# Kernel optimization log

Hardware: AMD Instinct MI355X
Metric: run time of the kernel (lower is better)

The kernel has to match this reference:

```python
import jax, jax.numpy as jnp
import numpy as np
import math

B, L, D, H = 4, 2048, 1024, 16
HD = D // H


def setup_inputs() -> dict:
    key = jax.random.key(0)
    k1, k2, k3 = jax.random.split(key, 3)
    x = jax.random.normal(k1, (B, L, D), dtype=jnp.float32)
    # Linear weights stored as [in, out] so y = x @ W (equivalent to torch x @ W.T)
    Wqkv = jax.random.normal(k2, (D, 3 * D), dtype=jnp.float32) * (1.0 / math.sqrt(D))
    Wproj = jax.random.normal(k3, (D, D), dtype=jnp.float32) * (1.0 / math.sqrt(D))
    attn_mask = jnp.tril(jnp.ones((L, L), dtype=bool))  # True = attend (causal)
    key_padding_mask = jnp.zeros((B, L), dtype=bool)     # True = padded (none here)
    return {"x": x, "Wqkv": Wqkv, "Wproj": Wproj,
            "attn_mask": attn_mask, "key_padding_mask": key_padding_mask}


def reference(x, Wqkv, Wproj, attn_mask, key_padding_mask):
    Bx, Lx, Dx = x.shape
    qkv = x @ Wqkv                              # [B, L, 3D]
    q, k, v = jnp.split(qkv, 3, axis=-1)
    def shape(t):
        return t.reshape(Bx, Lx, H, HD).transpose(0, 2, 1, 3)  # [B, H, L, hd]
    q, k, v = shape(q), shape(k), shape(v)
    att = jnp.einsum('bhqd,bhkd->bhqk', q, k) / math.sqrt(HD)  # [B, H, L, L]
    neg_inf = jnp.float32(-jnp.inf)
    att = jnp.where(attn_mask[None, None, :, :], att, neg_inf)
    att = jnp.where(key_padding_mask[:, None, None, :], neg_inf, att)
    att = jax.nn.softmax(att, axis=-1)
    y = jnp.einsum('bhqk,bhkd->bhqd', att, v)   # [B, H, L, hd]
    y = y.transpose(0, 2, 1, 3).reshape(Bx, Lx, Dx)
    return y @ Wproj
```

## Files before the change

### kernel.cpp

```cpp
#include <hip/hip_runtime.h>
#include <cstdint>
#include <cstddef>


typedef __attribute__((ext_vector_type(8))) __bf16 bf16x8;
typedef __attribute__((ext_vector_type(4))) __bf16 bf16x4;
typedef __attribute__((ext_vector_type(4))) float f32x4;
typedef __attribute__((ext_vector_type(16))) float f32x16;

__device__ __forceinline__ f32x4 mfma_bf16(bf16x8 a, bf16x8 b, f32x4 c) {
  return __builtin_amdgcn_mfma_f32_16x16x32_bf16(a, b, c, 0, 0, 0);
}

__device__ __forceinline__ f32x16 mfma32(bf16x8 a, bf16x8 b, f32x16 c) {
  return __builtin_amdgcn_mfma_f32_32x32x16_bf16(a, b, c, 0, 0, 0);
}

__device__ __forceinline__ unsigned cvtpk(float a, float b) {
  unsigned r;
  asm("v_cvt_pk_bf16_f32 %0, %1, %2" : "=v"(r) : "v"(a), "v"(b));
  return r;
}

__device__ __forceinline__ void async_copy16(const void* gsrc, void* ldsdst) {
  __builtin_amdgcn_global_load_lds(
      (const __attribute__((address_space(1))) void*)gsrc,
      (__attribute__((address_space(3))) void*)ldsdst, 16, 0, 0);
}

__global__ __launch_bounds__(256) void f32_to_bf16(
    const float* __restrict__ in, __bf16* __restrict__ out) {
  const size_t i = ((size_t)blockIdx.x * 256 + threadIdx.x) * 4;
  const float4 v = *(const float4*)&in[i];
  bf16x4 o = {(__bf16)v.x, (__bf16)v.y, (__bf16)v.z, (__bf16)v.w};
  *(bf16x4*)&out[i] = o;
}

__global__ __launch_bounds__(256) void transpose_f32_bf16(
    const float* __restrict__ in, __bf16* __restrict__ out, int R, int C) {
  __shared__ float tile[32][33];
  const int c0 = blockIdx.x * 32;
  const int r0 = blockIdx.y * 32;
  const int tx = threadIdx.x & 31;
  const int ty = threadIdx.x >> 5;
#pragma unroll
  for (int i = 0; i < 32; i += 8)
    tile[ty + i][tx] = in[(size_t)(r0 + ty + i) * C + c0 + tx];
  __syncthreads();
#pragma unroll
  for (int i = 0; i < 32; i += 8)
    out[(size_t)(c0 + ty + i) * R + r0 + tx] = (__bf16)tile[tx][ty + i];
}

__global__ __launch_bounds__(256) void gemm_bt_f32out(
    const __bf16* __restrict__ A, const __bf16* __restrict__ BT,
    float* __restrict__ C, int M, int N, int K) {
  __shared__ __bf16 As[128 * 32];
  __shared__ __bf16 Bs[128 * 32];
  const int tid = threadIdx.x;
  const int wave = tid >> 6;
  const int lane = tid & 63;
  const int n16 = lane & 15;
  const int quad = lane >> 4;
  const int m0 = blockIdx.x * 128;
  const int n0 = blockIdx.y * 128;
  const int wr = wave >> 1;
  const int wc = wave & 1;

  const f32x4 zero = {0.f, 0.f, 0.f, 0.f};
  f32x4 acc[4][4];
#pragma unroll
  for (int i = 0; i < 4; ++i)
#pragma unroll
    for (int j = 0; j < 4; ++j) acc[i][j] = zero;

  const int KT = K >> 5;
  for (int kt = 0; kt < KT; ++kt) {
    const int k0 = kt << 5;
#pragma unroll
    for (int r = 0; r < 2; ++r) {
      const int li = (r << 8) + tid;
      const int row = li >> 2;
      const int kp8 = (li & 3) << 3;
      const int lbase = ((r << 8) + (wave << 6)) << 3;
      async_copy16(&A[(size_t)(m0 + row) * K + k0 + kp8], &As[lbase]);
      async_copy16(&BT[(size_t)(n0 + row) * K + k0 + kp8], &Bs[lbase]);
    }
    __syncthreads();
    bf16x8 af[4], bf[4];
#pragma unroll
    for (int t = 0; t < 4; ++t) {
      af[t] = *(const bf16x8*)&As[(wr * 64 + t * 16 + n16) * 32 + quad * 8];
      bf[t] = *(const bf16x8*)&Bs[(wc * 64 + t * 16 + n16) * 32 + quad * 8];
    }
#pragma unroll
    for (int mt = 0; mt < 4; ++mt)
#pragma unroll
      for (int nt = 0; nt < 4; ++nt)
        acc[mt][nt] = mfma_bf16(af[mt], bf[nt], acc[mt][nt]);
    __syncthreads();
  }
#pragma unroll
  for (int mt = 0; mt < 4; ++mt) {
#pragma unroll
    for (int r = 0; r < 4; ++r) {
      const int m = m0 + wr * 64 + mt * 16 + quad * 4 + r;
#pragma unroll
      for (int nt = 0; nt < 4; ++nt) {
        const int n = n0 + wc * 64 + nt * 16 + n16;
        C[(size_t)m * N + n] = acc[mt][nt][r];
      }
    }
  }
}

__global__ __launch_bounds__(512, 2) void gemm_qkv(
    const __bf16* __restrict__ A, const __bf16* __restrict__ BT,
    __bf16* __restrict__ Q, __bf16* __restrict__ Kh, __bf16* __restrict__ VT) {
  extern __shared__ __bf16 smem[];
  const int K = 1024;
  const int wg = (blockIdx.x & 7) * 48 + (blockIdx.x >> 3);
  const int bm = wg / 12;
  const int bn = wg % 12;
  const int m0 = bm << 8;
  const int n0 = bn << 8;

  const int tid = threadIdx.x;
  const int wave = tid >> 6;
  const int lane = tid & 63;
  const int n16 = lane & 15;
  const int quad = lane >> 4;
  const int wr = wave >> 2;
  const int wc = wave & 3;

  const int srow = wave * 8 + (lane >> 3);
  const int schunk = ((lane & 7) ^ ((lane >> 3) & 7)) << 3;
  const __bf16* aS = &A[(size_t)(m0 + srow) * K + schunk];
  const __bf16* bS = &BT[(size_t)(n0 + srow) * K + schunk];
  __bf16* dstW = smem + wave * 512;

  const f32x4 zero = {0.f, 0.f, 0.f, 0.f};
  f32x4 acc[8][4];
#pragma unroll
  for (int i = 0; i < 8; ++i)
#pragma unroll
    for (int j = 0; j < 4; ++j) acc[i][j] = zero;

#pragma unroll
  for (int i = 0; i < 4; ++i) {
    async_copy16(aS + (size_t)i * 65536, dstW + i * 4096);
    async_copy16(bS + (size_t)i * 65536, dstW + 16384 + i * 4096);
  }

  for (int t = 0; t < 16; ++t) {
    const int base = (t & 1) << 15;
    asm volatile("s_waitcnt vmcnt(0)" ::: "memory");
    __builtin_amdgcn_s_barrier();
    if (t + 1 < 16) {
      const int nbase = ((t + 1) & 1) << 15;
      const __bf16* aT = aS + (t + 1) * 64;
      const __bf16* bT = bS + (t + 1) * 64;
#pragma unroll
      for (int i = 0; i < 4; ++i) {
        async_copy16(aT + (size_t)i * 65536, dstW + nbase + i * 4096);
        async_copy16(bT + (size_t)i * 65536, dstW + nbase + 16384 + i * 4096);
      }
    }
    const __bf16* As = smem + base;
    const __bf16* Bs = smem + base + 16384;
    bf16x8 bfr[4][2];
#pragma unroll
    for (int g = 0; g < 4; ++g)
#pragma unroll
      for (int kk = 0; kk < 2; ++kk) {
        const int row = wc * 64 + g * 16 + n16;
        const int phys = ((kk * 4 + quad) ^ (n16 & 7)) << 3;
        bfr[g][kk] = *(const bf16x8*)&Bs[row * 64 + phys];
      }
#pragma unroll
    for (int q = 0; q < 4; ++q) {
      bf16x8 afr[2][2];
#pragma unroll
      for (int fi = 0; fi < 2; ++fi)
#pragma unroll
        for (int kk = 0; kk < 2; ++kk) {
          const int row = wr * 128 + (2 * q + fi) * 16 + n16;
          const int phys = ((kk * 4 + quad) ^ (n16 & 7)) << 3;
          afr[fi][kk] = *(const bf16x8*)&As[row * 64 + phys];
        }
      __builtin_amdgcn_s_barrier();
      asm volatile("s_waitcnt lgkmcnt(0)" ::: "memory");
      __builtin_amdgcn_sched_barrier(0);
      __builtin_amdgcn_s_setprio(1);
#pragma unroll
      for (int fi = 0; fi < 2; ++fi)
#pragma unroll
        for (int g = 0; g < 4; ++g)
#pragma unroll
          for (int kk = 0; kk < 2; ++kk)
            acc[2 * q + fi][g] =
                mfma_bf16(afr[fi][kk], bfr[g][kk], acc[2 * q + fi][g]);
      __builtin_amdgcn_s_setprio(0);
      __builtin_amdgcn_s_barrier();
    }
  }

  __bf16* tw = smem + wave * 2048;
  const int b = m0 >> 11;
  const int l0w = (m0 & 2047) + wr * 128;
  const int n = n0 + wc * 64;

  if (n < 2048) {
    const float QSCALE = 0.125f * 1.44269504089f;
    const bool isQ = (n < 1024);
    const int h = (n & 1023) >> 6;
    __bf16* dst = isQ ? Q : Kh;
    const size_t bbase = ((size_t)(b * 16 + h) * 2048) * 64;
#pragma unroll
    for (int p = 0; p < 4; ++p) {
#pragma unroll
      for (int fi = 0; fi < 2; ++fi) {
        const int f = 2 * p + fi;
#pragma unroll
        for (int g = 0; g < 4; ++g)
#pragma unroll
          for (int r = 0; r < 4; ++r) {
            const int hd = g * 16 + n16;
            const int mm = fi * 16 + quad * 4 + r;
            const float v = isQ ? acc[f][g][r] * QSCALE : acc[f][g][r];
            tw[mm * 64 + (((hd >> 3) ^ (mm & 7)) << 3) + (hd & 7)] =
                (__bf16)v;
          }
      }
#pragma unroll
      for (int i = 0; i < 4; ++i) {
        const int c = lane + 64 * i;
        const int row = c >> 3;
        const int hd0 = (c & 7) << 3;
        const int phys = (c & 7) ^ (row & 7);
        const bf16x8 v = *(const bf16x8*)&tw[row * 64 + phys * 8];
        *(bf16x8*)&dst[bbase + (size_t)(l0w + p * 32 + row) * 64 + hd0] = v;
      }
    }
  } else {
    const int h = (n - 2048) >> 6;
    const size_t bhead = (size_t)(b * 16 + h);
#pragma unroll
    for (int ph = 0; ph < 2; ++ph)
#pragma unroll
      for (int lh = 0; lh < 2; ++lh) {
#pragma unroll
        for (int gi = 0; gi < 2; ++gi) {
          const int g = 2 * ph + gi;
#pragma unroll
          for (int fi = 0; fi < 4; ++fi) {
            const int f = 4 * lh + fi;
#pragma unroll
            for (int r = 0; r < 4; ++r) {
              const int hdp = gi * 16 + n16;
              const int mm = fi * 16 + quad * 4 + r;
              const int phys = (mm >> 3) ^ (hdp & 7);
              tw[hdp * 64 + phys * 8 + (mm & 7)] = (__bf16)acc[f][g][r];
            }
          }
        }
#pragma unroll
        for (int i = 0; i < 4; ++i) {
          const int c = lane + 64 * i;
          const int row = c >> 3;
          const int phys = (c & 7) ^ (row & 7);
          const bf16x8 v = *(const bf16x8*)&tw[row * 64 + phys * 8];
          *(bf16x8*)&VT[(bhead * 64 + ph * 32 + row) * 2048 + l0w + lh * 64 +
                        (c & 7) * 8] = v;
        }
      }
  }
}

__global__ __launch_bounds__(256, 2) void flash_attn(
    const __bf16* __restrict__ Q, const __bf16* __restrict__ Kh,
    const __bf16* __restrict__ VT, __bf16* __restrict__ Y) {
  __shared__ __bf16 Ks[2][64 * 64];
  __shared__ __bf16 Vs[2][64 * 64];
  const int bh = blockIdx.x;
  const int p = blockIdx.y;
  const int tid = threadIdx.x;
  const int wave = tid >> 6;
  const int lane = tid & 63;
  const int lrow = lane & 31;
  const int hi = lane >> 5;
  const int lswz = lane & 7;
  const __bf16* Qb = Q + (size_t)bh * 2048 * 64;
  const __bf16* Kb = Kh + (size_t)bh * 2048 * 64;
  const __bf16* Vb = VT + (size_t)bh * 64 * 2048;
  const int b = bh >> 4;
  const int h = bh & 15;
  const f32x16 zero16 = {0.f, 0.f, 0.f, 0.f, 0.f, 0.f, 0.f, 0.f,
                         0.f, 0.f, 0.f, 0.f, 0.f, 0.f, 0.f, 0.f};

  const int srow = tid >> 3;
  const int sswz = ((tid & 7) ^ (srow & 7)) << 3;
  const size_t kg0 = (size_t)srow * 64 + sswz;
  const size_t kg1 = (size_t)(srow + 32) * 64 + sswz;
  const size_t vg0 = (size_t)srow * 2048 + sswz;
  const size_t vg1 = (size_t)(srow + 32) * 2048 + sswz;
  const int ldst0 = wave * 512;
  const int ldst1 = 2048 + wave * 512;

#pragma unroll
  for (int tt = 0; tt < 2; ++tt) {
    const int t = tt ? 15 - p : p;
    const int q0w = t * 128 + wave * 32;
    const int myq = q0w + lrow;

    bf16x8 qf[4];
#pragma unroll
    for (int i = 0; i < 4; ++i)
      qf[i] = *(const bf16x8*)&Qb[(size_t)myq * 64 + i * 16 + hi * 8];

    f32x16 o0 = zero16, o1 = zero16;
    float lsum = 0.f;
    const int nsteps = 2 * (t + 1);

    __syncthreads();
    async_copy16(&Kb[kg0], &Ks[0][ldst0]);
    async_copy16(&Kb[kg1], &Ks[0][ldst1]);
    async_copy16(&Vb[vg0], &Vs[0][ldst0]);
    async_copy16(&Vb[vg1], &Vs[0][ldst1]);

    for (int kt = 0; kt < nsteps; ++kt) {
      const int buf = kt & 1;
      const int c0 = kt << 6;
      __syncthreads();
      if (kt + 1 < nsteps) {
        const int nb = buf ^ 1;
        const int cn = c0 + 64;
        async_copy16(&Kb[kg0 + (size_t)cn * 64], &Ks[nb][ldst0]);
        async_copy16(&Kb[kg1 + (size_t)cn * 64], &Ks[nb][ldst1]);
        async_copy16(&Vb[vg0 + cn], &Vs[nb][ldst0]);
        async_copy16(&Vb[vg1 + cn], &Vs[nb][ldst1]);
      }
      if (c0 > q0w + 31) continue;

      const __bf16* ks = Ks[buf];
      const __bf16* vs = Vs[buf];

      f32x16 sc[2];
#pragma unroll
      for (int ch = 0; ch < 2; ++ch) {
        sc[ch] = zero16;
#pragma unroll
        for (int i = 0; i < 4; ++i) {
          const bf16x8 kf = *(const bf16x8*)&ks[(ch * 32 + lrow) * 64 +
                                                (((2 * i + hi) ^ lswz) << 3)];
          sc[ch] = mfma32(kf, qf[i], sc[ch]);
        }
      }
      if (c0 + 63 > q0w) {
#pragma unroll
        for (int ch = 0; ch < 2; ++ch)
#pragma unroll
          for (int r = 0; r < 16; ++r) {
            const int k = c0 + ch * 32 + (r & 3) + 8 * (r >> 2) + 4 * hi;
            float e = __builtin_amdgcn_exp2f(sc[ch][r]);
            e = (k <= myq) ? e : 0.f;
            sc[ch][r] = e;
            lsum += e;
          }
      } else {
#pragma unroll
        for (int ch = 0; ch < 2; ++ch)
#pragma unroll
          for (int r = 0; r < 16; ++r) {
            const float e = __builtin_amdgcn_exp2f(sc[ch][r]);
            sc[ch][r] = e;
            lsum += e;
          }
      }
#pragma unroll
      for (int ch = 0; ch < 2; ++ch) {
#pragma unroll
        for (int kc = 0; kc < 2; ++kc) {
          unsigned c01 = cvtpk(sc[ch][kc * 8 + 0], sc[ch][kc * 8 + 1]);
          unsigned c23 = cvtpk(sc[ch][kc * 8 + 2], sc[ch][kc * 8 + 3]);
          unsigned c45 = cvtpk(sc[ch][kc * 8 + 4], sc[ch][kc * 8 + 5]);
          unsigned c67 = cvtpk(sc[ch][kc * 8 + 6], sc[ch][kc * 8 + 7]);
          asm("v_permlane32_swap_b32 %0, %1" : "+v"(c01), "+v"(c45));
          asm("v_permlane32_swap_b32 %0, %1" : "+v"(c23), "+v"(c67));
          union {
            unsigned u[4];
            bf16x8 v;
          } pu;
          pu.u[0] = c01;
          pu.u[1] = c23;
          pu.u[2] = c45;
          pu.u[3] = c67;
          const int kch = ch * 4 + kc * 2 + hi;
          {
            const bf16x8 vf0 = *(const bf16x8*)&vs[(0 * 32 + lrow) * 64 +
                                                   ((kch ^ lswz) << 3)];
            o0 = mfma32(pu.v, vf0, o0);
            const bf16x8 vf1 = *(const bf16x8*)&vs[(1 * 32 + lrow) * 64 +
                                                   ((kch ^ lswz) << 3)];
            o1 = mfma32(pu.v, vf1, o1);
          }
        }
      }
    }

    lsum += __shfl_xor(lsum, 32);
    const float inv = 1.0f / lsum;
    float invr[16];
#pragma unroll
    for (int r = 0; r < 16; ++r)
      invr[r] = __shfl(inv, (r & 3) + 8 * (r >> 2) + 4 * hi);
#pragma unroll
    for (int r = 0; r < 16; ++r) {
      const int row = q0w + (r & 3) + 8 * (r >> 2) + 4 * hi;
      const size_t yb = (size_t)(b * 2048 + row) * 1024 + h * 64;
      Y[yb + lrow] = (__bf16)(o0[r] * invr[r]);
      Y[yb + 32 + lrow] = (__bf16)(o1[r] * invr[r]);
    }
  }
}

extern "C" void kernel_launch(void* const* d_in, const int* in_sizes, int n_in,
                              void* d_out, int out_size, void* d_ws,
                              size_t ws_size, hipStream_t stream) {
  const float* x = (const float*)d_in[0];
  const float* Wqkv = (const float*)d_in[1];
  const float* Wproj = (const float*)d_in[2];
  float* out = (float*)d_out;

  char* ws = (char*)d_ws;
  __bf16* xb = (__bf16*)ws;     ws += (size_t)8192 * 1024 * 2;
  __bf16* WqkvT = (__bf16*)ws;  ws += (size_t)3072 * 1024 * 2;
  __bf16* WprojT = (__bf16*)ws; ws += (size_t)1024 * 1024 * 2;
  __bf16* Qs = (__bf16*)ws;     ws += (size_t)64 * 2048 * 64 * 2;
  __bf16* Ks = (__bf16*)ws;     ws += (size_t)64 * 2048 * 64 * 2;
  __bf16* VTs = (__bf16*)ws;    ws += (size_t)64 * 64 * 2048 * 2;
  __bf16* attn = xb;

  static bool attrSet = false;
  if (!attrSet) {
    hipFuncSetAttribute((const void*)gemm_qkv,
                        hipFuncAttributeMaxDynamicSharedMemorySize, 131072);
    attrSet = true;
  }

  f32_to_bf16<<<8192, 256, 0, stream>>>(x, xb);
  transpose_f32_bf16<<<dim3(96, 32), 256, 0, stream>>>(Wqkv, WqkvT, 1024, 3072);
  transpose_f32_bf16<<<dim3(32, 32), 256, 0, stream>>>(Wproj, WprojT, 1024, 1024);
  gemm_qkv<<<384, 512, 131072, stream>>>(xb, WqkvT, Qs, Ks, VTs);
  flash_attn<<<dim3(64, 8), 256, 0, stream>>>(Qs, Ks, VTs, attn);
  gemm_bt_f32out<<<dim3(64, 8), 256, 0, stream>>>(attn, WprojT, out,
                                                  8192, 1024, 1024);
}
```

Measured before the change: 253.1 us.

## Interleave global-to-LDS prefetch with MFMA phases in QKV GEMM main loop

```diff
diff --git a/kernel.cpp b/kernel.cpp
--- a/kernel.cpp
+++ b/kernel.cpp
@@ -114,6 +114,40 @@
   }
 }
 
+#define DS_B(Bs_)                                                            \
+  _Pragma("unroll") for (int g = 0; g < 4; ++g)                              \
+      _Pragma("unroll") for (int kk = 0; kk < 2; ++kk) bfr[g][kk] =          \
+          *(const bf16x8*)&(Bs_)[(wc * 64 + g * 16 + n16) * 64 +             \
+                                 (((kk * 4 + quad) ^ (n16 & 7)) << 3)];
+
+#define DS_A2(As_, q_)                                                       \
+  _Pragma("unroll") for (int fi = 0; fi < 2; ++fi)                           \
+      _Pragma("unroll") for (int kk = 0; kk < 2; ++kk) af[fi][kk] =          \
+          *(const bf16x8*)&(As_)[(wr * 128 + (2 * (q_) + fi) * 16 + n16) *   \
+                                     64 +                                    \
+                                 (((kk * 4 + quad) ^ (n16 & 7)) << 3)];
+
+#define MFMA_BODY(q_)                                                        \
+  __builtin_amdgcn_s_barrier();                                              \
+  asm volatile("s_waitcnt lgkmcnt(0)" ::: "memory");                         \
+  __builtin_amdgcn_sched_barrier(0);                                         \
+  __builtin_amdgcn_s_setprio(1);                                             \
+  _Pragma("unroll") for (int fi = 0; fi < 2; ++fi)                           \
+      _Pragma("unroll") for (int g = 0; g < 4; ++g)                          \
+          _Pragma("unroll") for (int kk = 0; kk < 2; ++kk)                   \
+              acc[2 * (q_) + fi][g] =                                        \
+      mfma_bf16(af[fi][kk], bfr[g][kk], acc[2 * (q_) + fi][g]);              \
+  __builtin_amdgcn_s_setprio(0);
+
+#define MFMA_PH(q_)                                                          \
+  MFMA_BODY(q_)                                                              \
+  __builtin_amdgcn_s_barrier();
+
+#define MFMA_PH_VM(q_)                                                       \
+  MFMA_BODY(q_)                                                              \
+  asm volatile("s_waitcnt vmcnt(6)" ::: "memory");                           \
+  __builtin_amdgcn_s_barrier();
+
 __global__ __launch_bounds__(512, 2) void gemm_qkv(
     const __bf16* __restrict__ A, const __bf16* __restrict__ BT,
     __bf16* __restrict__ Q, __bf16* __restrict__ Kh, __bf16* __restrict__ VT) {
@@ -133,11 +167,19 @@
   const int wr = wave >> 2;
   const int wc = wave & 3;
 
-  const int srow = wave * 8 + (lane >> 3);
-  const int schunk = ((lane & 7) ^ ((lane >> 3) & 7)) << 3;
-  const __bf16* aS = &A[(size_t)(m0 + srow) * K + schunk];
-  const __bf16* bS = &BT[(size_t)(n0 + srow) * K + schunk];
-  __bf16* dstW = smem + wave * 512;
+  const int srow = tid >> 3;
+  const int schunk = ((tid & 7) ^ (srow & 7)) << 3;
+  const __bf16* aBase = &A[(size_t)(m0 + srow) * K + schunk];
+  const __bf16* bBase = &BT[(size_t)(n0 + srow) * K + schunk];
+
+  auto stgA = [&](int kt, int u, int half) {
+    async_copy16(aBase + (size_t)u * 65536 + kt * 64,
+                 smem + half * 32768 + u * 4096 + wave * 512);
+  };
+  auto stgB = [&](int kt, int u, int half) {
+    async_copy16(bBase + (size_t)u * 65536 + kt * 64,
+                 smem + half * 32768 + 16384 + u * 4096 + wave * 512);
+  };
 
   const f32x4 zero = {0.f, 0.f, 0.f, 0.f};
   f32x4 acc[8][4];
@@ -146,64 +188,54 @@
 #pragma unroll
     for (int j = 0; j < 4; ++j) acc[i][j] = zero;
 
-#pragma unroll
-  for (int i = 0; i < 4; ++i) {
-    async_copy16(aS + (size_t)i * 65536, dstW + i * 4096);
-    async_copy16(bS + (size_t)i * 65536, dstW + 16384 + i * 4096);
-  }
-
-  for (int t = 0; t < 16; ++t) {
-    const int base = (t & 1) << 15;
-    asm volatile("s_waitcnt vmcnt(0)" ::: "memory");
-    __builtin_amdgcn_s_barrier();
-    if (t + 1 < 16) {
-      const int nbase = ((t + 1) & 1) << 15;
-      const __bf16* aT = aS + (t + 1) * 64;
-      const __bf16* bT = bS + (t + 1) * 64;
-#pragma unroll
-      for (int i = 0; i < 4; ++i) {
-        async_copy16(aT + (size_t)i * 65536, dstW + nbase + i * 4096);
-        async_copy16(bT + (size_t)i * 65536, dstW + nbase + 16384 + i * 4096);
-      }
-    }
-    const __bf16* As = smem + base;
-    const __bf16* Bs = smem + base + 16384;
-    bf16x8 bfr[4][2];
-#pragma unroll
-    for (int g = 0; g < 4; ++g)
-#pragma unroll
-      for (int kk = 0; kk < 2; ++kk) {
-        const int row = wc * 64 + g * 16 + n16;
-        const int phys = ((kk * 4 + quad) ^ (n16 & 7)) << 3;
-        bfr[g][kk] = *(const bf16x8*)&Bs[row * 64 + phys];
-      }
-#pragma unroll
-    for (int q = 0; q < 4; ++q) {
-      bf16x8 afr[2][2];
-#pragma unroll
-      for (int fi = 0; fi < 2; ++fi)
-#pragma unroll
-        for (int kk = 0; kk < 2; ++kk) {
-          const int row = wr * 128 + (2 * q + fi) * 16 + n16;
-          const int phys = ((kk * 4 + quad) ^ (n16 & 7)) << 3;
-          afr[fi][kk] = *(const bf16x8*)&As[row * 64 + phys];
-        }
-      __builtin_amdgcn_s_barrier();
-      asm volatile("s_waitcnt lgkmcnt(0)" ::: "memory");
-      __builtin_amdgcn_sched_barrier(0);
-      __builtin_amdgcn_s_setprio(1);
-#pragma unroll
-      for (int fi = 0; fi < 2; ++fi)
-#pragma unroll
-        for (int g = 0; g < 4; ++g)
-#pragma unroll
-          for (int kk = 0; kk < 2; ++kk)
-            acc[2 * q + fi][g] =
-                mfma_bf16(afr[fi][kk], bfr[g][kk], acc[2 * q + fi][g]);
-      __builtin_amdgcn_s_setprio(0);
-      __builtin_amdgcn_s_barrier();
-    }
-  }
+  const __bf16* As0 = smem;
+  const __bf16* Bs0 = smem + 16384;
+  const __bf16* As1 = smem + 32768;
+  const __bf16* Bs1 = smem + 49152;
+
+  stgB(0, 0, 0); stgB(0, 1, 0); stgB(0, 2, 0); stgB(0, 3, 0);
+  stgA(0, 0, 0); stgA(0, 2, 0); stgA(0, 1, 0); stgA(0, 3, 0);
+  stgB(1, 0, 1); stgB(1, 1, 1); stgB(1, 2, 1); stgB(1, 3, 1);
+  stgA(1, 0, 1); stgA(1, 2, 1);
+  asm volatile("s_waitcnt vmcnt(6)" ::: "memory");
+  __builtin_amdgcn_s_barrier();
+
+  for (int t = 0; t < 8; ++t) {
+    const int knE = (2 * t + 2) & 15;
+    const int knO = (2 * t + 3) & 15;
+    bf16x8 bfr[4][2], af[2][2];
+
+    DS_B(Bs0)
+    DS_A2(As0, 0)
+    stgA(2 * t + 1, 1, 1); stgA(2 * t + 1, 3, 1);
+    asm volatile("s_waitcnt lgkmcnt(8)" ::: "memory");
+    MFMA_PH(0)
+    DS_A2(As0, 1)
+    stgB(knE, 0, 0); stgB(knE, 1, 0);
+    MFMA_PH(1)
+    DS_A2(As0, 2)
+    stgB(knE, 2, 0); stgB(knE, 3, 0);
+    MFMA_PH(2)
+    DS_A2(As0, 3)
+    stgA(knE, 0, 0); stgA(knE, 2, 0);
+    MFMA_PH_VM(3)
+    DS_B(Bs1)
+    DS_A2(As1, 0)
+    stgA(knE, 1, 0); stgA(knE, 3, 0);
+    asm volatile("s_waitcnt lgkmcnt(8)" ::: "memory");
+    MFMA_PH(0)
+    DS_A2(As1, 1)
+    stgB(knO, 0, 1); stgB(knO, 1, 1);
+    MFMA_PH(1)
+    DS_A2(As1, 2)
+    stgB(knO, 2, 1); stgB(knO, 3, 1);
+    MFMA_PH(2)
+    DS_A2(As1, 3)
+    stgA(knO, 0, 1); stgA(knO, 2, 1);
+    MFMA_PH_VM(3)
+  }
+  asm volatile("s_waitcnt vmcnt(0)" ::: "memory");
+  __builtin_amdgcn_s_barrier();
 
   __bf16* tw = smem + wave * 2048;
   const int b = m0 >> 11;
@@ -241,6 +273,7 @@
         const bf16x8 v = *(const bf16x8*)&tw[row * 64 + phys * 8];
         *(bf16x8*)&dst[bbase + (size_t)(l0w + p * 32 + row) * 64 + hd0] = v;
       }
+      __builtin_amdgcn_s_barrier();
     }
   } else {
     const int h = (n - 2048) >> 6;
@@ -273,6 +306,7 @@
           *(bf16x8*)&VT[(bhead * 64 + ph * 32 + row) * 2048 + l0w + lh * 64 +
                         (c & 7) * 8] = v;
         }
+        __builtin_amdgcn_s_barrier();
       }
   }
 }
```

Result: no change. 248.8 us (-1.7%).
